# Kernel tuning notes

Hardware: AMD Instinct MI355X
Metric: run time of the kernel (lower is better)

Reference implementation:

```python
import jax, jax.numpy as jnp
import numpy as np

N, M, D = 1024, 1024, 512


def setup_inputs() -> dict:
    key = jax.random.key(0)
    ks = jax.random.split(key, 12)
    s = 1.0 / np.sqrt(D)
    return {
        "q": jax.random.normal(ks[0], (N, D), jnp.float32),
        "k": jax.random.normal(ks[1], (M, D), jnp.float32),
        "v": jax.random.normal(ks[2], (M, D), jnp.float32),
        "mask": jax.random.randint(ks[3], (N, M), 0, 2) > 0,
        "Wq": jax.random.normal(ks[4], (D, D), jnp.float32) * s,
        "bq": jax.random.normal(ks[5], (D,), jnp.float32) * s,
        "Wk": jax.random.normal(ks[6], (D, D), jnp.float32) * s,
        "bk": jax.random.normal(ks[7], (D,), jnp.float32) * s,
        "Wv": jax.random.normal(ks[8], (D, D), jnp.float32) * s,
        "bv": jax.random.normal(ks[9], (D,), jnp.float32) * s,
        "Ww": jax.random.normal(ks[10], (D,), jnp.float32) * s,
        "bw": jax.random.normal(ks[11], (1,), jnp.float32) * s,
    }


def reference(q, k, v, mask, Wq, bq, Wk, bk, Wv, bv, Ww, bw):
    # Linear projections (torch Linear: x @ W.T + b)
    qp = q @ Wq.T + bq  # [N, D]
    kp = k @ Wk.T + bk  # [M, D]
    vp = v @ Wv.T + bv  # [M, D]
    # Bahdanau additive score: W(tanh(q_n + k_m)) -> [N, M]
    h = jnp.tanh(qp[:, None, :] + kp[None, :, :])  # [N, M, D]
    scores = jnp.einsum('nmd,d->nm', h, Ww) + bw[0]
    scores = jnp.where(mask, scores, jnp.float32(-1000000.0))
    attn = jax.nn.softmax(scores, axis=1)  # softmax over M (dim 1)
    context = jnp.einsum('nm,md->nd', attn, vp)  # [N, D]
    return context
```

## Files before the change

kernel.cpp:

```cpp
#include <hip/hip_runtime.h>
#include <hip/hip_bf16.h>
#include <float.h>


#define NROWS 1024
#define DDIM  512
#define MDIM  1024

typedef __attribute__((ext_vector_type(8))) short s8v;
typedef __attribute__((ext_vector_type(4))) float f4v;
typedef __attribute__((ext_vector_type(2))) float v2f;

__device__ __forceinline__ float bf2f(ushort h) {
    return __uint_as_float(((unsigned)h) << 16);
}
__device__ __forceinline__ ushort2 f2bf2(float a, float b) {
    __hip_bfloat162 t = __float22bfloat162_rn(float2{a, b});
    union { __hip_bfloat162 v; ushort2 u; } c; c.v = t;
    return c.u;
}
__device__ __forceinline__ void hl2(float a, float b, ushort2& h, ushort2& l) {
    h = f2bf2(a, b);
    l = f2bf2(a - bf2f(h.x), b - bf2f(h.y));
}

__device__ __forceinline__ void load_lds16(const float* g, float* l) {
    __builtin_amdgcn_global_load_lds(
        (const __attribute__((address_space(1))) void*)g,
        (__attribute__((address_space(3))) void*)l, 16, 0, 0);
}

__global__ __launch_bounds__(256) void proj_gemm(
    const float* __restrict__ q, const float* __restrict__ kk_,
    const float* __restrict__ v,
    const float* __restrict__ Wq, const float* __restrict__ bq,
    const float* __restrict__ Wk, const float* __restrict__ bk,
    const float* __restrict__ Wv, const float* __restrict__ bv,
    float* __restrict__ eq, float* __restrict__ ekT,
    ushort* __restrict__ vph, ushort* __restrict__ vpl,
    float* __restrict__ S, float CS)
{
    __shared__ ushort Ah[4096], Al[4096], Bh[4096], Bl[4096];

    const float* A; const float* B; const float* bias;
    int biasRow;
    if (blockIdx.z == 0)      { A = q;   B = Wq;  bias = bq; biasRow = 0; }
    else if (blockIdx.z == 1) { A = Wk;  B = kk_; bias = bk; biasRow = 1; }
    else                      { A = Wv;  B = v;   bias = bv; biasRow = 1; }

    const int bi = (blockIdx.z == 0) ? blockIdx.x : blockIdx.y;
    const int bj = (blockIdx.z == 0) ? blockIdx.y : blockIdx.x;

    const int t    = threadIdx.x;
    const int lane = t & 63;
    const int w    = t >> 6;
    const int lm   = lane & 15;
    const int lq   = lane >> 4;
    const int i0   = bi * 64;
    const int j0   = bj * 64;
    const int mh   = (w >> 1) * 32;
    const int nh   = (w & 1) * 32;

    if (blockIdx.z == 0) {
        const int jb = blockIdx.x * 8 + blockIdx.y;
        float4 zz = {0.f, 0.f, 0.f, 0.f};
#pragma unroll
        for (int p = 0; p < 8; ++p)
            *(float4*)&S[(size_t)jb * 8192 + (t + p * 256) * 4] = zz;
    }

    f4v acc[2][2] = {{{0.f,0.f,0.f,0.f},{0.f,0.f,0.f,0.f}},
                     {{0.f,0.f,0.f,0.f},{0.f,0.f,0.f,0.f}}};
    float4 pa[4], pb[4];

    const int sr = t >> 4, sc4 = t & 15;
#pragma unroll
    for (int p = 0; p < 4; ++p) {
        int r = sr + p * 16;
        pa[p] = *(const float4*)&A[(size_t)(i0 + r) * DDIM + sc4 * 4];
        pb[p] = *(const float4*)&B[(size_t)(j0 + r) * DDIM + sc4 * 4];
    }

    for (int kc = 0; kc < 8; ++kc) {
        __syncthreads();
#pragma unroll
        for (int p = 0; p < 4; ++p) {
            int r = sr + p * 16;
            int ad = r * 64 + (((sc4 >> 1) ^ (r & 7)) << 3) + (sc4 & 1) * 4;
            ushort2 h01, l01, h23, l23;
            hl2(pa[p].x, pa[p].y, h01, l01);
            hl2(pa[p].z, pa[p].w, h23, l23);
            ushort4 ha = {h01.x, h01.y, h23.x, h23.y};
            ushort4 la = {l01.x, l01.y, l23.x, l23.y};
            *(ushort4*)&Ah[ad] = ha;
            *(ushort4*)&Al[ad] = la;
            hl2(pb[p].x, pb[p].y, h01, l01);
            hl2(pb[p].z, pb[p].w, h23, l23);
            ushort4 hb = {h01.x, h01.y, h23.x, h23.y};
            ushort4 lb = {l01.x, l01.y, l23.x, l23.y};
            *(ushort4*)&Bh[ad] = hb;
            *(ushort4*)&Bl[ad] = lb;
        }
        __syncthreads();
        if (kc < 7) {
            const int k0 = (kc + 1) * 64;
#pragma unroll
            for (int p = 0; p < 4; ++p) {
                int r = sr + p * 16;
                pa[p] = *(const float4*)&A[(size_t)(i0 + r) * DDIM + k0 + sc4 * 4];
                pb[p] = *(const float4*)&B[(size_t)(j0 + r) * DDIM + k0 + sc4 * 4];
            }
        }
#pragma unroll
        for (int ks = 0; ks < 2; ++ks) {
            const int kb = ks * 4 + lq;
            s8v afh[2], afl[2], bfh[2], bfl[2];
#pragma unroll
            for (int g = 0; g < 2; ++g) {
                int ra = mh + g * 16 + lm;
                int rb = nh + g * 16 + lm;
                int aa = ra * 64 + ((kb ^ (ra & 7)) << 3);
                int ab = rb * 64 + ((kb ^ (rb & 7)) << 3);
                afh[g] = *(const s8v*)&Ah[aa];
                afl[g] = *(const s8v*)&Al[aa];
                bfh[g] = *(const s8v*)&Bh[ab];
                bfl[g] = *(const s8v*)&Bl[ab];
            }
#pragma unroll
            for (int mi = 0; mi < 2; ++mi)
#pragma unroll
                for (int ni = 0; ni < 2; ++ni) {
                    acc[mi][ni] = __builtin_amdgcn_mfma_f32_16x16x32_bf16(
                        afh[mi], bfh[ni], acc[mi][ni], 0, 0, 0);
                    acc[mi][ni] = __builtin_amdgcn_mfma_f32_16x16x32_bf16(
                        afh[mi], bfl[ni], acc[mi][ni], 0, 0, 0);
                    acc[mi][ni] = __builtin_amdgcn_mfma_f32_16x16x32_bf16(
                        afl[mi], bfh[ni], acc[mi][ni], 0, 0, 0);
                }
        }
    }

    const float CLAMP = 8192.0f;
#pragma unroll
    for (int mi = 0; mi < 2; ++mi) {
#pragma unroll
        for (int ni = 0; ni < 2; ++ni) {
#pragma unroll
            for (int p = 0; p < 4; ++p) {
                int row = i0 + mh + mi * 16 + lq * 4 + p;
                int col = j0 + nh + ni * 16 + lm;
                float val = acc[mi][ni][p] + (biasRow ? bias[row] : bias[col]);
                if (blockIdx.z == 0) {
                    eq[(size_t)row * 512 + col] =
                        fminf(__builtin_amdgcn_exp2f(val * CS), CLAMP);
                } else if (blockIdx.z == 1) {
                    ekT[(size_t)row * 1024 + col] =
                        fminf(__builtin_amdgcn_exp2f(val * CS), CLAMP);
                } else {
                    ushort2 h2 = f2bf2(val, val);
                    vph[(size_t)row * 1024 + col] = h2.x;
                    ushort2 l2 = f2bf2(val - bf2f(h2.x), 0.f);
                    vpl[(size_t)row * 1024 + col] = l2.x;
                }
            }
        }
    }
}

#define DCH  32
#define SMCH 128
__global__ __launch_bounds__(256) void score_kernel(const float* __restrict__ eq,
                                                    const float* __restrict__ ekT,
                                                    const float* __restrict__ Ww,
                                                    float* __restrict__ S)
{
    __shared__ __align__(16) float ks[DCH * SMCH];
    __shared__ __align__(16) float es[16 * 128];
    __shared__ __align__(16) float wws[128];
    const int t    = threadIdx.x;
    const int lane = t & 63;
    const int w    = t >> 6;
    const int m0   = blockIdx.x * SMCH;
    const int n0   = blockIdx.y * 16;
    const int dbase = blockIdx.z * 128;

    const float SC = 1.220703125e-4f;

#pragma unroll
    for (int p = 0; p < 2; ++p) {
        int idx = t + p * 256;
        int nl = idx >> 5, dd4 = idx & 31;
        float4 e4 = *(const float4*)&eq[(size_t)(n0 + nl) * DDIM + dbase + dd4 * 4];
        float4 e4s = {e4.x * SC, e4.y * SC, e4.z * SC, e4.w * SC};
        *(float4*)&es[nl * 128 + dd4 * 4] = e4s;
    }
    if (t < 128) wws[t] = Ww[dbase + t] * SC;

    v2f acc[4] = {};
    const v2f cc2 = {1.220703125e-4f, 1.220703125e-4f};

    for (int dc = 0; dc < 128; dc += DCH) {
        const int d0 = dbase + dc;
        __syncthreads();
#pragma unroll
        for (int i = 0; i < 4; ++i) {
            int r2 = w * 8 + i * 2;
            const float* g = ekT + (size_t)(d0 + r2 + (lane >> 5)) * MDIM
                             + m0 + (lane & 31) * 4;
            load_lds16(g, &ks[r2 * SMCH]);
        }
        __syncthreads();

#pragma unroll
        for (int dq = 0; dq < DCH; dq += 8) {
            v2f k0 = *(const v2f*)&ks[(dq + 0) * SMCH + lane * 2];
            v2f k1 = *(const v2f*)&ks[(dq + 1) * SMCH + lane * 2];
            v2f k2 = *(const v2f*)&ks[(dq + 2) * SMCH + lane * 2];
            v2f k3 = *(const v2f*)&ks[(dq + 3) * SMCH + lane * 2];
            v2f k4 = *(const v2f*)&ks[(dq + 4) * SMCH + lane * 2];
            v2f k5 = *(const v2f*)&ks[(dq + 5) * SMCH + lane * 2];
            v2f k6 = *(const v2f*)&ks[(dq + 6) * SMCH + lane * 2];
            v2f k7 = *(const v2f*)&ks[(dq + 7) * SMCH + lane * 2];
            float4 wgA = *(const float4*)&wws[dc + dq];
            float4 wgB = *(const float4*)&wws[dc + dq + 4];
#pragma unroll
            for (int nn = 0; nn < 4; ++nn) {
                float4 egA = *(const float4*)&es[(w * 4 + nn) * 128 + dc + dq];
                float4 egB = *(const float4*)&es[(w * 4 + nn) * 128 + dc + dq + 4];
                v2f A0 = __builtin_elementwise_fma(k0, (v2f){egA.x, egA.x}, cc2);
                v2f A1 = __builtin_elementwise_fma(k1, (v2f){egA.y, egA.y}, cc2);
                v2f A2 = __builtin_elementwise_fma(k2, (v2f){egA.z, egA.z}, cc2);
                v2f A3 = __builtin_elementwise_fma(k3, (v2f){egA.w, egA.w}, cc2);
                v2f A4 = __builtin_elementwise_fma(k4, (v2f){egB.x, egB.x}, cc2);
                v2f A5 = __builtin_elementwise_fma(k5, (v2f){egB.y, egB.y}, cc2);
                v2f A6 = __builtin_elementwise_fma(k6, (v2f){egB.z, egB.z}, cc2);
                v2f A7 = __builtin_elementwise_fma(k7, (v2f){egB.w, egB.w}, cc2);
                v2f n01 = __builtin_elementwise_fma((v2f){wgA.y, wgA.y}, A0,
                                                    (v2f){wgA.x, wgA.x} * A1);
                v2f d01 = A0 * A1;
                v2f n23 = __builtin_elementwise_fma((v2f){wgA.w, wgA.w}, A2,
                                                    (v2f){wgA.z, wgA.z} * A3);
                v2f d23 = A2 * A3;
                v2f n45 = __builtin_elementwise_fma((v2f){wgB.y, wgB.y}, A4,
                                                    (v2f){wgB.x, wgB.x} * A5);
                v2f d45 = A4 * A5;
                v2f n67 = __builtin_elementwise_fma((v2f){wgB.w, wgB.w}, A6,
                                                    (v2f){wgB.z, wgB.z} * A7);
                v2f d67 = A6 * A7;
                v2f nA = __builtin_elementwise_fma(n01, d23, n23 * d01);
                v2f dA = d01 * d23;
                v2f nB = __builtin_elementwise_fma(n45, d67, n67 * d45);
                v2f dB = d45 * d67;
                v2f num = __builtin_elementwise_fma(nA, dB, nB * dA);
                v2f den = dA * dB;
                v2f r = {__builtin_amdgcn_rcpf(den.x), __builtin_amdgcn_rcpf(den.y)};
                acc[nn] = __builtin_elementwise_fma(num, r, acc[nn]);
            }
        }
    }

    const float C2 = -2.8853900817779268f;
    const int m = m0 + lane * 2;
#pragma unroll
    for (int nn = 0; nn < 4; ++nn) {
        int n = n0 + w * 4 + nn;
        atomicAdd(&S[(size_t)n * MDIM + m],     acc[nn].x * C2);
        atomicAdd(&S[(size_t)n * MDIM + m + 1], acc[nn].y * C2);
    }
}

__global__ __launch_bounds__(256) void combine_kernel(const float* __restrict__ S,
                                                      const int* __restrict__ mask,
                                                      ushort* __restrict__ Ph,
                                                      ushort* __restrict__ Pl,
                                                      float* __restrict__ rsum)
{
    __shared__ float red[4];
    const int n = blockIdx.x, t = threadIdx.x;
    const int lane = t & 63, w = t >> 6;

    float4 s  = *(const float4*)&S[(size_t)n * MDIM + t * 4];
    int4   mk = *(const int4*)&mask[(size_t)n * MDIM + t * 4];
    float p0 = mk.x ? __builtin_amdgcn_exp2f(s.x) : 0.f;
    float p1 = mk.y ? __builtin_amdgcn_exp2f(s.y) : 0.f;
    float p2 = mk.z ? __builtin_amdgcn_exp2f(s.z) : 0.f;
    float p3 = mk.w ? __builtin_amdgcn_exp2f(s.w) : 0.f;

    ushort2 h01, l01, h23, l23;
    hl2(p0, p1, h01, l01);
    hl2(p2, p3, h23, l23);
    ushort4 hv = {h01.x, h01.y, h23.x, h23.y};
    ushort4 lv = {l01.x, l01.y, l23.x, l23.y};
    *(ushort4*)&Ph[(size_t)n * MDIM + t * 4] = hv;
    *(ushort4*)&Pl[(size_t)n * MDIM + t * 4] = lv;

    float rs = (p0 + p1) + (p2 + p3);
#pragma unroll
    for (int off = 32; off; off >>= 1) rs += __shfl_xor(rs, off);
    if (lane == 0) red[w] = rs;
    __syncthreads();
    if (t == 0) rsum[n] = (red[0] + red[1]) + (red[2] + red[3]);
}

__global__ __launch_bounds__(256) void ctx_gemm(const ushort* __restrict__ Ph,
                                                const ushort* __restrict__ Pl,
                                                const ushort* __restrict__ vph,
                                                const ushort* __restrict__ vpl,
                                                const float* __restrict__ rsum,
                                                float* __restrict__ out)
{
    const int t    = threadIdx.x;
    const int lane = t & 63;
    const int w    = t >> 6;
    const int lm   = lane & 15;
    const int lq   = lane >> 4;
    const int d0   = blockIdx.x * 64 + w * 16;
    const int n0   = blockIdx.y * 16;

    const ushort* pAh = Ph  + (size_t)(n0 + lm) * MDIM + lq * 8;
    const ushort* pAl = Pl  + (size_t)(n0 + lm) * MDIM + lq * 8;
    const ushort* pBh = vph + (size_t)(d0 + lm) * MDIM + lq * 8;
    const ushort* pBl = vpl + (size_t)(d0 + lm) * MDIM + lq * 8;

    f4v acc = {0.f, 0.f, 0.f, 0.f};
#pragma unroll 4
    for (int m0 = 0; m0 < MDIM; m0 += 32) {
        s8v ah = *(const s8v*)(pAh + m0);
        s8v al = *(const s8v*)(pAl + m0);
        s8v bh = *(const s8v*)(pBh + m0);
        s8v bl = *(const s8v*)(pBl + m0);
        acc = __builtin_amdgcn_mfma_f32_16x16x32_bf16(ah, bh, acc, 0, 0, 0);
        acc = __builtin_amdgcn_mfma_f32_16x16x32_bf16(ah, bl, acc, 0, 0, 0);
        acc = __builtin_amdgcn_mfma_f32_16x16x32_bf16(al, bh, acc, 0, 0, 0);
    }

#pragma unroll
    for (int p = 0; p < 4; ++p) {
        int nrow = n0 + lq * 4 + p;
        float inv = __builtin_amdgcn_rcpf(rsum[nrow]);
        out[(size_t)nrow * DDIM + d0 + lm] = acc[p] * inv;
    }
}

extern "C" void kernel_launch(void* const* d_in, const int* in_sizes, int n_in,
                              void* d_out, int out_size, void* d_ws, size_t ws_size,
                              hipStream_t stream)
{
    const float* q    = (const float*)d_in[0];
    const float* k    = (const float*)d_in[1];
    const float* v    = (const float*)d_in[2];
    const int*   mask = (const int*)d_in[3];
    const float* Wq   = (const float*)d_in[4];
    const float* bq   = (const float*)d_in[5];
    const float* Wk   = (const float*)d_in[6];
    const float* bk   = (const float*)d_in[7];
    const float* Wv   = (const float*)d_in[8];
    const float* bv   = (const float*)d_in[9];
    const float* Ww   = (const float*)d_in[10];

    float* ws    = (float*)d_ws;
    float* eq    = ws;
    float* ekT   = ws + 524288;
    ushort* vph  = (ushort*)(ws + 1048576);
    ushort* vpl  = (ushort*)(ws + 1310720);
    float* S     = ws + 1572864;
    float* rsum  = ws + 2621440;
    ushort* Ph   = (ushort*)ws;
    ushort* Pl   = (ushort*)(ws + 524288);
    float* out   = (float*)d_out;

    const float CS = 2.8853900817779268f;

    proj_gemm<<<dim3(16, 8, 3), dim3(256), 0, stream>>>(q, k, v, Wq, bq, Wk, bk,
                                                        Wv, bv, eq, ekT,
                                                        vph, vpl, S, CS);
    score_kernel<<<dim3(8, 64, 4), dim3(256), 0, stream>>>(eq, ekT, Ww, S);
    combine_kernel<<<dim3(1024), dim3(256), 0, stream>>>(S, mask, Ph, Pl, rsum);
    ctx_gemm<<<dim3(8, 64), dim3(256), 0, stream>>>(Ph, Pl, vph, vpl, rsum, out);
}
```

Before: 177.5 us.

## Fuse softmax combine into score kernel via last-block atomic counter

Each score tile is now reduced over four D-chunk blocks, and a per-tile atomic counter picks the last block to finish. That block reads the finished S tile, applies the mask and exp2, writes the bf16 hi/lo P values and accumulates row sums atomically. This drops the separate combine kernel launch and its extra pass over S. In exchange the score kernel pays an extra counter atomic per block and a serialized tail in the last-arriving blocks. The path only runs when the workspace is large enough to hold the separate P buffers.

Result: slower. 203.3 us (+14.6%).

```diff
diff --git a/kernel.cpp b/kernel.cpp
--- a/kernel.cpp
+++ b/kernel.cpp
@@ -38,7 +38,8 @@
     const float* __restrict__ Wv, const float* __restrict__ bv,
     float* __restrict__ eq, float* __restrict__ ekT,
     ushort* __restrict__ vph, ushort* __restrict__ vpl,
-    float* __restrict__ S, float CS)
+    float* __restrict__ S, float* __restrict__ rsum, int* __restrict__ cnt,
+    int fused, float CS)
 {
     __shared__ ushort Ah[4096], Al[4096], Bh[4096], Bl[4096];
 
@@ -67,6 +68,10 @@
 #pragma unroll
         for (int p = 0; p < 8; ++p)
             *(float4*)&S[(size_t)jb * 8192 + (t + p * 256) * 4] = zz;
+        if (fused && jb == 0) {
+            *(float4*)&rsum[t * 4] = zz;
+            if (t < 128) *(int4*)&cnt[t * 4] = int4{0, 0, 0, 0};
+        }
     }
 
     f4v acc[2][2] = {{{0.f,0.f,0.f,0.f},{0.f,0.f,0.f,0.f}},
@@ -172,11 +177,18 @@
 __global__ __launch_bounds__(256) void score_kernel(const float* __restrict__ eq,
                                                     const float* __restrict__ ekT,
                                                     const float* __restrict__ Ww,
-                                                    float* __restrict__ S)
+                                                    const int* __restrict__ mask,
+                                                    float* __restrict__ S,
+                                                    ushort* __restrict__ Ph,
+                                                    ushort* __restrict__ Pl,
+                                                    float* __restrict__ rsum,
+                                                    int* __restrict__ cnt,
+                                                    int fused)
 {
     __shared__ __align__(16) float ks[DCH * SMCH];
     __shared__ __align__(16) float es[16 * 128];
     __shared__ __align__(16) float wws[128];
+    __shared__ int lastflag;
     const int t    = threadIdx.x;
     const int lane = t & 63;
     const int w    = t >> 6;
@@ -267,6 +279,47 @@
         atomicAdd(&S[(size_t)n * MDIM + m],     acc[nn].x * C2);
         atomicAdd(&S[(size_t)n * MDIM + m + 1], acc[nn].y * C2);
     }
+
+    if (!fused) return;
+
+    __syncthreads();
+    if (t == 0) {
+        int old = __hip_atomic_fetch_add(&cnt[blockIdx.y * 8 + blockIdx.x], 1,
+                                         __ATOMIC_ACQ_REL,
+                                         __HIP_MEMORY_SCOPE_AGENT);
+        lastflag = (old == 3);
+    }
+    __syncthreads();
+    if (!lastflag) return;
+
+    const int nl = t >> 4;
+    const int f0 = t & 15;
+#pragma unroll
+    for (int g = 0; g < 2; ++g) {
+        int f = f0 + g * 16;
+        size_t base = (size_t)(n0 + nl) * MDIM + m0 + f * 4;
+        float sv[4];
+#pragma unroll
+        for (int e = 0; e < 4; ++e)
+            sv[e] = __hip_atomic_load(&S[base + e], __ATOMIC_RELAXED,
+                                      __HIP_MEMORY_SCOPE_AGENT);
+        int4 mk = *(const int4*)&mask[base];
+        float p0 = mk.x ? __builtin_amdgcn_exp2f(sv[0]) : 0.f;
+        float p1 = mk.y ? __builtin_amdgcn_exp2f(sv[1]) : 0.f;
+        float p2 = mk.z ? __builtin_amdgcn_exp2f(sv[2]) : 0.f;
+        float p3 = mk.w ? __builtin_amdgcn_exp2f(sv[3]) : 0.f;
+        ushort2 h01, l01, h23, l23;
+        hl2(p0, p1, h01, l01);
+        hl2(p2, p3, h23, l23);
+        ushort4 hv = {h01.x, h01.y, h23.x, h23.y};
+        ushort4 lv = {l01.x, l01.y, l23.x, l23.y};
+        *(ushort4*)&Ph[base] = hv;
+        *(ushort4*)&Pl[base] = lv;
+        float rs = (p0 + p1) + (p2 + p3);
+#pragma unroll
+        for (int off = 1; off < 16; off <<= 1) rs += __shfl_xor(rs, off);
+        if ((lane & 15) == 0) atomicAdd(&rsum[n0 + nl], rs);
+    }
 }
 
 __global__ __launch_bounds__(256) void combine_kernel(const float* __restrict__ S,
@@ -364,17 +417,32 @@
     ushort* vph  = (ushort*)(ws + 1048576);
     ushort* vpl  = (ushort*)(ws + 1310720);
     float* S     = ws + 1572864;
-    float* rsum  = ws + 2621440;
-    ushort* Ph   = (ushort*)ws;
-    ushort* Pl   = (ushort*)(ws + 524288);
     float* out   = (float*)d_out;
+
+    const int fused = (ws_size >= (size_t)3671552 * 4);
+    ushort* Ph; ushort* Pl; float* rsum; int* cnt;
+    if (fused) {
+        Ph   = (ushort*)(ws + 2621440);
+        Pl   = (ushort*)(ws + 3145728);
+        rsum = ws + 3670016;
+        cnt  = (int*)(ws + 3671040);
+    } else {
+        Ph   = (ushort*)ws;
+        Pl   = (ushort*)(ws + 524288);
+        rsum = ws + 2621440;
+        cnt  = (int*)(ws + 2621952);
+    }
 
     const float CS = 2.8853900817779268f;
 
     proj_gemm<<<dim3(16, 8, 3), dim3(256), 0, stream>>>(q, k, v, Wq, bq, Wk, bk,
                                                         Wv, bv, eq, ekT,
-                                                        vph, vpl, S, CS);
-    score_kernel<<<dim3(8, 64, 4), dim3(256), 0, stream>>>(eq, ekT, Ww, S);
-    combine_kernel<<<dim3(1024), dim3(256), 0, stream>>>(S, mask, Ph, Pl, rsum);
+                                                        vph, vpl, S, rsum, cnt,
+                                                        fused, CS);
+    score_kernel<<<dim3(8, 64, 4), dim3(256), 0, stream>>>(eq, ekT, Ww, mask, S,
+                                                           Ph, Pl, rsum, cnt,
+                                                           fused);
+    if (!fused)
+        combine_kernel<<<dim3(1024), dim3(256), 0, stream>>>(S, mask, Ph, Pl, rsum);
     ctx_gemm<<<dim3(8, 64), dim3(256), 0, stream>>>(Ph, Pl, vph, vpl, rsum, out);
 }
```
